# Performance work log

Hardware: AMD Instinct MI355X
Metric: run time of the kernel (lower is better)

The kernel has to match this reference:

```python
import jax, jax.numpy as jnp
from jax import lax
import numpy as np

L, B, D, H = 256, 128, 512, 512


def setup_inputs() -> dict:
    rng = np.random.default_rng(0)
    # random projective-ish dependency trees: node 0 is root, head[i] < i
    heads = np.full((B, L), -1, dtype=np.int64)
    for i in range(1, L):
        heads[:, i] = rng.integers(0, i, size=B)
    # bottom-up traversal order (children have larger index than parent)
    indexes = np.tile(np.arange(L - 1, -1, -1, dtype=np.int32)[:, None], (1, B))  # [L,B]
    # cm_full[b,p,j] = 1 if j is a child of p in tree b
    cm_full = (heads[:, None, :] == np.arange(L)[None, :, None]).astype(np.float32)  # [B,L,L]
    child_mask = cm_full[:, ::-1, :].transpose(1, 0, 2).copy()  # [L,B,L] aligned with indexes
    # top-down order: root first (ascending index works since head[i] < i)
    td_node = np.tile(np.arange(L, dtype=np.int32)[:, None], (1, B))  # [L,B]
    td_parent_idx = np.maximum(heads.T, 0).astype(np.int32)  # [L,B]
    td_parent_valid = (heads.T >= 0).astype(np.float32)  # [L,B], 0 at root
    root_index = np.zeros(B, dtype=np.int32)

    key = jax.random.key(0)
    ks = jax.random.split(key, 7)
    sx = 1.0 / np.sqrt(D)
    sh = 1.0 / np.sqrt(H)
    return {
        "emb": jax.random.normal(ks[0], (L, B, D), jnp.float32),
        "indexes": jnp.asarray(indexes),
        "child_mask": jnp.asarray(child_mask),
        "td_node": jnp.asarray(td_node),
        "td_parent_idx": jnp.asarray(td_parent_idx),
        "td_parent_valid": jnp.asarray(td_parent_valid),
        "root_index": jnp.asarray(root_index),
        "dt_Wx": jax.random.normal(ks[1], (D, 3 * H), jnp.float32) * sx,
        "dt_Uh": jax.random.normal(ks[2], (H, 3 * H), jnp.float32) * sh,
        "dt_b": jnp.zeros((3 * H,), jnp.float32),
        "td_Wx": jax.random.normal(ks[3], (D, 3 * H), jnp.float32) * sx,
        "td_Uh": jax.random.normal(ks[4], (H, 3 * H), jnp.float32) * sh,
        "td_b": jnp.zeros((3 * H,), jnp.float32),
    }


def _gru_cell(x, h, Wx, Uh, b):
    # standard GRU: gates laid out as [r, z, n]
    xg = x @ Wx + b
    hg = h @ Uh
    xr, xz, xn = jnp.split(xg, 3, axis=-1)
    hr, hz, hn = jnp.split(hg, 3, axis=-1)
    r = jax.nn.sigmoid(xr + hr)
    z = jax.nn.sigmoid(xz + hz)
    n = jnp.tanh(xn + r * hn)
    return (1.0 - z) * n + z * h


def reference(emb, indexes, child_mask, td_node, td_parent_idx, td_parent_valid,
              root_index, dt_Wx, dt_Uh, dt_b, td_Wx, td_Uh, td_b):
    Ld, Bd, Dd = emb.shape
    Hd = dt_Uh.shape[0]
    barange = jnp.arange(Bd)

    # ---- bottom-up (DT) pass: h_prev = sum of children hiddens ----
    x_dt = jnp.take_along_axis(emb, indexes[:, :, None], axis=0)  # [L,B,D]

    def dt_step(Hs, xs):
        x, node, cmask = xs                      # [B,D], [B], [B,L]
        h = jnp.einsum('bl,blh->bh', cmask, Hs)  # sum over children
        hn = _gru_cell(x, h, dt_Wx, dt_Uh, dt_b)
        return Hs.at[barange, node].set(hn), None

    Hdt, _ = lax.scan(dt_step, jnp.zeros((Bd, Ld, Hd), emb.dtype),
                      (x_dt, indexes, child_mask))

    # ---- top-down (TD) pass: h_prev = parent hidden (zeros at root) ----
    x_td = jnp.take_along_axis(emb, td_node[:, :, None], axis=0)  # [L,B,D]

    def td_step(Hs, xs):
        x, node, pidx, pvalid = xs
        h = Hs[barange, pidx] * pvalid[:, None]
        hn = _gru_cell(x, h, td_Wx, td_Uh, td_b)
        return Hs.at[barange, node].set(hn), None

    Htd, _ = lax.scan(td_step, jnp.zeros((Bd, Ld, Hd), emb.dtype),
                      (x_td, td_node, td_parent_idx, td_parent_valid))

    outputs = jnp.concatenate([Hdt, Htd], axis=-1)  # [B,L,2H] (batch-first as original)
    root_h = jnp.concatenate([Hdt[barange, root_index], Htd[barange, root_index]], axis=-1)
    output_t = root_h[None]  # [1,B,2H]
    return outputs, output_t
```

## Files before the change

kernel.cpp:

```cpp
#include <hip/hip_runtime.h>


#define NL 256
#define NB 128
#define NH 512
#define NG (NB * NL)

typedef short short8 __attribute__((ext_vector_type(8)));
typedef float f32x4 __attribute__((ext_vector_type(4)));

__device__ __forceinline__ float bf2f(unsigned short u) {
  union { unsigned int i; float f; } c; c.i = ((unsigned int)u) << 16; return c.f;
}
__device__ __forceinline__ unsigned short f2bf(float f) {
  union { float f; unsigned int i; } c; c.f = f;
  return (unsigned short)((c.i + 0x7FFFu + ((c.i >> 16) & 1u)) >> 16);
}
__device__ __forceinline__ short8 pk_bf16(f32x4 a, f32x4 b) {
  union { unsigned int u[4]; short8 s; } r;
  asm("v_cvt_pk_bf16_f32 %0, %1, %2" : "=v"(r.u[0]) : "v"(a[0]), "v"(a[1]));
  asm("v_cvt_pk_bf16_f32 %0, %1, %2" : "=v"(r.u[1]) : "v"(a[2]), "v"(a[3]));
  asm("v_cvt_pk_bf16_f32 %0, %1, %2" : "=v"(r.u[2]) : "v"(b[0]), "v"(b[1]));
  asm("v_cvt_pk_bf16_f32 %0, %1, %2" : "=v"(r.u[3]) : "v"(b[2]), "v"(b[3]));
  return r.s;
}
__device__ __forceinline__ void atom_pk_bf16(unsigned short* p, unsigned int ud) {
  asm volatile("global_atomic_pk_add_bf16 %0, %1, off" :: "v"((void*)p), "v"(ud) : "memory");
}

__device__ __forceinline__ void level_wait(unsigned int* c, unsigned int target) {
  if (threadIdx.x == 0) {
    while (__hip_atomic_load(c, __ATOMIC_RELAXED, __HIP_MEMORY_SCOPE_AGENT) < target)
      __builtin_amdgcn_s_sleep(8);
  }
  __syncthreads();
  __builtin_amdgcn_fence(__ATOMIC_ACQUIRE, "agent");
}

__global__ void prep_wt4(const float* __restrict__ w0, const float* __restrict__ w1,
                         const float* __restrict__ w2, const float* __restrict__ w3,
                         unsigned short* __restrict__ wt) {
  __shared__ float t[32][33];
  const float* w = blockIdx.z == 0 ? w0 : blockIdx.z == 1 ? w1 : blockIdx.z == 2 ? w2 : w3;
  unsigned short* dst = wt + (size_t)blockIdx.z * 1536 * 512;
  int n0 = blockIdx.x * 32, k0 = blockIdx.y * 32;
  int tx = threadIdx.x & 31, ty = threadIdx.x >> 5;
  #pragma unroll
  for (int i = 0; i < 4; ++i)
    t[ty + 8 * i][tx] = w[(size_t)(k0 + ty + 8 * i) * 1536 + n0 + tx];
  __syncthreads();
  #pragma unroll
  for (int i = 0; i < 4; ++i)
    dst[(size_t)(n0 + ty + 8 * i) * 512 + k0 + tx] = f2bf(t[tx][ty + 8 * i]);
}

__global__ void prep_sched(const int* __restrict__ td_pidx,
                           const float* __restrict__ td_pval,
                           int* __restrict__ sched, int* __restrict__ meta,
                           int* __restrict__ gidx, int* __restrict__ pslot) {
  __shared__ unsigned char dep[NB][NL];
  __shared__ unsigned short cnb[NB][256];
  __shared__ int cnt[256];
  __shared__ int off[257];
  __shared__ int dmax_s;
  const int tid = threadIdx.x;
  for (int j = tid; j < NB * 256; j += 256) ((unsigned short*)cnb)[j] = 0;
  if (tid == 0) dmax_s = 0;
  __syncthreads();
  if (tid < NB) {
    int b = tid, lmax = 0;
    for (int i = 0; i < NL; ++i) {
      float pv = td_pval[i * NB + b];
      int pi = td_pidx[i * NB + b];
      int d = (pv != 0.f) ? (int)dep[b][pi] + 1 : 0;
      dep[b][i] = (unsigned char)d;
      cnb[b][d]++;
      lmax = max(lmax, d);
    }
    atomicMax(&dmax_s, lmax);
  }
  __syncthreads();
  {
    int s = 0;
    for (int b = 0; b < NB; ++b) s += cnb[b][tid];
    cnt[tid] = s;
  }
  __syncthreads();
  if (tid == 0) {
    int s = 0;
    for (int d = 0; d < 256; ++d) { off[d] = s; s += cnt[d]; }
    off[256] = s;
  }
  __syncthreads();
  {
    int run = off[tid];
    for (int b = 0; b < NB; ++b) {
      int t = cnb[b][tid];
      cnb[b][tid] = (unsigned short)run;
      run += t;
    }
  }
  __syncthreads();
  if (tid < NB) {
    int b = tid;
    for (int i = 0; i < NL; ++i) {
      float pv = td_pval[i * NB + b];
      int pi = td_pidx[i * NB + b];
      int d = dep[b][i];
      int g = cnb[b][d]++;
      sched[g] = (b << 8) | i;
      gidx[b * NL + i] = g;
      pslot[g] = (pv != 0.f) ? gidx[b * NL + pi] : -1;
    }
  }
  if (tid == 0) meta[0] = dmax_s;
  __syncthreads();
  meta[1 + tid] = off[tid];
  meta[257 + tid] = cnt[tid];
}

__global__ void prep_xc(const float* __restrict__ emb, const int* __restrict__ sched,
                        unsigned short* __restrict__ Xc) {
  int g = blockIdx.x * 4 + (threadIdx.x >> 6);
  int lane = threadIdx.x & 63;
  int e = sched[g];
  int b = e >> 8, node = e & 255;
  const float* src = emb + ((size_t)node * NB + b) * 512 + lane * 8;
  f32x4 v0 = *(const f32x4*)src;
  f32x4 v1 = *(const f32x4*)(src + 4);
  *(short8*)(Xc + (size_t)g * 512 + lane * 8) = pk_bf16(v0, v1);
}

__launch_bounds__(512, 2)
__global__ void tree_gru(const float* __restrict__ dt_b,
                         const float* __restrict__ td_b,
                         const unsigned short* __restrict__ wt,
                         const unsigned short* __restrict__ Xc,
                         unsigned short* __restrict__ Hdt,
                         unsigned short* __restrict__ Htd,
                         unsigned short* __restrict__ Hfd,
                         const unsigned short* __restrict__ zrow,
                         const int* __restrict__ meta,
                         const int* __restrict__ pslot,
                         unsigned int* __restrict__ ctr,
                         const int* __restrict__ sched,
                         const int* __restrict__ root_index,
                         float* __restrict__ out) {
  extern __shared__ unsigned char lds[];
  const int tid = threadIdx.x;
  const int bi  = blockIdx.x;
  const int cg   = bi >> 3;
  const int pass = (bi >> 2) & 1;
  const int rep  = bi & 3;
  const int w  = tid >> 6, l = tid & 63;
  const int lm = l & 15, kg = l >> 4;
  const int col = cg * 16 + lm;

  for (int idx = tid; idx < 6144; idx += 512) {
    int k8  = idx & 63;
    int n   = (idx >> 6) & 15;
    int g   = (idx >> 10) % 3;
    int mat = idx / 3072;
    const unsigned short* src = wt + (size_t)(pass * 2 + mat) * (1536 * 512)
                                   + (size_t)(g * 512 + cg * 16 + n) * 512 + k8 * 8;
    short8 v = *(const short8*)src;
    int off = ((mat * 3 + g) * 16 + n) * 1024 + ((k8 * 16) ^ ((n & 7) << 4));
    *(short8*)(lds + off) = v;
  }
  unsigned char* Xb = lds + 98304;
  unsigned char* Hb = lds + 98304 + 16384;
  __syncthreads();

  const float* bias = pass ? td_b : dt_b;
  const float br = bias[col], bz = bias[NH + col], bn = bias[2 * NH + col];
  const int base_wr = (0 * 16 + lm) * 1024;
  const int base_wz = (1 * 16 + lm) * 1024;
  const int base_wn = (2 * 16 + lm) * 1024;
  const int base_ur = (3 * 16 + lm) * 1024;
  const int base_uz = (4 * 16 + lm) * 1024;
  const int base_un = (5 * 16 + lm) * 1024;
  const int wswz = (lm & 7) << 4;
  const int srow = tid >> 3, sslot = tid & 7;
  const int dsw = ((sslot ^ (srow & 7)) << 4);
  const int ck = cg >> 2;
  const int ccol2 = 2 * ((cg & 3) * 16 + lm);
  const int Dmax = meta[0];
  unsigned int* doneP = ctr + pass * 256;

  for (int p = 0; p <= Dmax; ++p) {
    const int d = pass ? p : (Dmax - p);
    const int off_d = meta[1 + d];
    const int cnt_d = meta[257 + d];
    const int T = (cnt_d + 127) >> 7;
    if (T <= rep) continue;
    const int dl = pass ? d - 1 : d + 1;
    if (dl >= 0 && dl <= Dmax)
      level_wait(doneP + dl, (unsigned int)meta[257 + dl] * 32u);
    for (int t = rep; t < T; t += 4) {
      const int g0 = off_d + t * 128;
      const int rows = min(128, cnt_d - t * 128);
      const unsigned short *sx[2], *sh[2];
      #pragma unroll
      for (int i = 0; i < 2; ++i) {
        int r = min(i * 64 + srow, rows - 1);
        int gg = g0 + r;
        sx[i] = Xc + (size_t)gg * 512 + sslot * 8;
        if (pass == 0) {
          sh[i] = Hdt + (size_t)gg * 512 + sslot * 8;
        } else {
          int ps = pslot[gg];
          sh[i] = (ps >= 0 ? Htd + (size_t)ps * 512 : zrow) + sslot * 8;
        }
      }
      const int c0 = (ck + 1) & 7;
      short8 rx0 = *(const short8*)(sx[0] + c0 * 64);
      short8 rx1 = *(const short8*)(sx[1] + c0 * 64);
      short8 rh0 = *(const short8*)(sh[0] + c0 * 64);
      short8 rh1 = *(const short8*)(sh[1] + c0 * 64);
      f32x4 aR = {0,0,0,0}, aZ = {0,0,0,0}, aXN = {0,0,0,0}, aHN = {0,0,0,0};
      #pragma unroll
      for (int ci = 0; ci < 8; ++ci) {
        const int c = (ck + 1 + ci) & 7;
        __syncthreads();
        *(short8*)(Xb + (srow)      * 128 + dsw) = rx0;
        *(short8*)(Xb + (64 + srow) * 128 + dsw) = rx1;
        *(short8*)(Hb + (srow)      * 128 + dsw) = rh0;
        *(short8*)(Hb + (64 + srow) * 128 + dsw) = rh1;
        if (ci < 7) {
          const int cn = (ck + 2 + ci) & 7;
          rx0 = *(const short8*)(sx[0] + cn * 64);
          rx1 = *(const short8*)(sx[1] + cn * 64);
          rh0 = *(const short8*)(sh[0] + cn * 64);
          rh1 = *(const short8*)(sh[1] + cn * 64);
        }
        __syncthreads();
        #pragma unroll
        for (int ks = 0; ks < 2; ++ks) {
          const int so = (((ks << 2) | kg) ^ (lm & 7)) << 4;
          const int arow = w * 16 + lm;
          short8 ax = *(const short8*)(Xb + arow * 128 + so);
          short8 ah = *(const short8*)(Hb + arow * 128 + so);
          const int kb = (c * 128 + ks * 64 + kg * 16) ^ wswz;
          short8 bwr = *(const short8*)(lds + base_wr + kb);
          short8 bwz = *(const short8*)(lds + base_wz + kb);
          short8 bwn = *(const short8*)(lds + base_wn + kb);
          short8 bur = *(const short8*)(lds + base_ur + kb);
          short8 buz = *(const short8*)(lds + base_uz + kb);
          short8 bun = *(const short8*)(lds + base_un + kb);
          aR  = __builtin_amdgcn_mfma_f32_16x16x32_bf16(ax, bwr, aR, 0, 0, 0);
          aZ  = __builtin_amdgcn_mfma_f32_16x16x32_bf16(ax, bwz, aZ, 0, 0, 0);
          aXN = __builtin_amdgcn_mfma_f32_16x16x32_bf16(ax, bwn, aXN, 0, 0, 0);
          aR  = __builtin_amdgcn_mfma_f32_16x16x32_bf16(ah, bur, aR, 0, 0, 0);
          aZ  = __builtin_amdgcn_mfma_f32_16x16x32_bf16(ah, buz, aZ, 0, 0, 0);
          aHN = __builtin_amdgcn_mfma_f32_16x16x32_bf16(ah, bun, aHN, 0, 0, 0);
        }
      }
      #pragma unroll
      for (int q = 0; q < 4; ++q) {
        const int r = w * 16 + kg * 4 + q;
        if (r >= rows) continue;
        const int g = g0 + r;
        const float hprev = bf2f(*(const unsigned short*)(
            Hb + r * 128 + (ccol2 ^ ((r & 7) << 4))));
        float rr = 1.f / (1.f + __expf(-(aR[q] + br)));
        float zz = 1.f / (1.f + __expf(-(aZ[q] + bz)));
        float e2 = __expf(2.f * (aXN[q] + bn + rr * aHN[q]));
        float nn = (e2 - 1.f) / (e2 + 1.f);
        float h = (1.f - zz) * nn + zz * hprev;
        float ho = __shfl_xor(h, 1);
        if (!(lm & 1)) {
          unsigned int ud;
          asm("v_cvt_pk_bf16_f32 %0, %1, %2" : "=v"(ud) : "v"(h), "v"(ho));
          if (pass == 0) {
            atom_pk_bf16(Hfd + (size_t)g * 512 + col, ud);
            int ps = pslot[g];
            if (ps >= 0) atom_pk_bf16(Hdt + (size_t)ps * 512 + col, ud);
          } else {
            atom_pk_bf16(Htd + (size_t)g * 512 + col, ud);
          }
        }
      }
      asm volatile("s_waitcnt vmcnt(0)" ::: "memory");
      __syncthreads();
      if (tid == 0) {
        __hip_atomic_fetch_add(doneP + d, (unsigned int)rows,
                               __ATOMIC_RELAXED, __HIP_MEMORY_SCOPE_AGENT);
        __hip_atomic_fetch_add(ctr + 512 + pass, (unsigned int)rows,
                               __ATOMIC_RELAXED, __HIP_MEMORY_SCOPE_AGENT);
      }
    }
  }

  level_wait(ctr + 512, (unsigned int)NG * 32u);
  level_wait(ctr + 513, (unsigned int)NG * 32u);
  #pragma unroll
  for (int it = 0; it < 4; ++it) {
    const int g = bi * 128 + it * 32 + (tid >> 4);
    const int part = tid & 15;
    const int e = sched[g];
    const int b = e >> 8, node = e & 255;
    float* dst = out + ((size_t)b * NL + node) * 1024;
    const bool isroot = (node == root_index[b]);
    float* dst2 = out + (size_t)NB * NL * 1024 + (size_t)b * 1024;
    const unsigned short* s1 = Hfd + (size_t)g * 512 + part * 32;
    const unsigned short* s2 = Htd + (size_t)g * 512 + part * 32;
    #pragma unroll
    for (int half = 0; half < 2; ++half) {
      const unsigned short* s = half ? s2 : s1;
      const int o = half * 512 + part * 32;
      #pragma unroll
      for (int j = 0; j < 4; ++j) {
        short8 v = *(const short8*)(s + j * 8);
        f32x4 lo, hi;
        #pragma unroll
        for (int q = 0; q < 4; ++q) {
          lo[q] = bf2f((unsigned short)v[q]);
          hi[q] = bf2f((unsigned short)v[4 + q]);
        }
        __builtin_nontemporal_store(lo, (f32x4*)(dst + o + j * 8));
        __builtin_nontemporal_store(hi, (f32x4*)(dst + o + j * 8 + 4));
        if (isroot) {
          *(f32x4*)(dst2 + o + j * 8) = lo;
          *(f32x4*)(dst2 + o + j * 8 + 4) = hi;
        }
      }
    }
  }
}

extern "C" void kernel_launch(void* const* d_in, const int* in_sizes, int n_in,
                              void* d_out, int out_size, void* d_ws, size_t ws_size,
                              hipStream_t stream) {
  (void)in_sizes; (void)n_in; (void)out_size; (void)ws_size;
  const float* emb      = (const float*)d_in[0];
  const int*   td_pidx  = (const int*)d_in[4];
  const float* td_pval  = (const float*)d_in[5];
  const int*   root_idx = (const int*)d_in[6];
  const float* dt_Wx    = (const float*)d_in[7];
  const float* dt_Uh    = (const float*)d_in[8];
  const float* dt_b     = (const float*)d_in[9];
  const float* td_Wx    = (const float*)d_in[10];
  const float* td_Uh    = (const float*)d_in[11];
  const float* td_b     = (const float*)d_in[12];
  float* out = (float*)d_out;

  unsigned short* wt   = (unsigned short*)d_ws;
  unsigned short* Xc   = wt + (size_t)4 * 1536 * 512;
  unsigned short* Hdt  = Xc + (size_t)NG * NH;
  unsigned short* Htd  = Hdt + (size_t)NG * NH;
  unsigned short* Hfd  = Htd + (size_t)NG * NH;
  unsigned short* zrow = Hfd + (size_t)NG * NH;
  unsigned int*   ctr  = (unsigned int*)(zrow + NH);
  int* sched = (int*)(ctr + 520);
  int* meta  = sched + NG;
  int* gidx  = meta + 520;
  int* pslot = gidx + NG;

  const size_t zbytes = (size_t)3 * NG * NH * 2 + NH * 2 + 520 * 4;
  (void)hipMemsetAsync(Hdt, 0, zbytes, stream);
  prep_wt4<<<dim3(48, 16, 4), dim3(256), 0, stream>>>(dt_Wx, dt_Uh, td_Wx, td_Uh, wt);
  prep_sched<<<dim3(1), dim3(256), 0, stream>>>(td_pidx, td_pval, sched, meta, gidx, pslot);
  prep_xc<<<dim3(NG / 4), dim3(256), 0, stream>>>(emb, sched, Xc);

  (void)hipFuncSetAttribute((const void*)tree_gru,
                            hipFuncAttributeMaxDynamicSharedMemorySize, 131072);

  void* args[] = {
    (void*)&dt_b, (void*)&td_b, (void*)&wt, (void*)&Xc, (void*)&Hdt, (void*)&Htd,
    (void*)&Hfd, (void*)&zrow, (void*)&meta, (void*)&pslot, (void*)&ctr,
    (void*)&sched, (void*)&root_idx, (void*)&out
  };
  (void)hipLaunchCooperativeKernel((const void*)tree_gru, dim3(256), dim3(512),
                                   args, 131072u, stream);
}
```

Before: 1.659 ms.

## Double row tile to 256 per block so each wave computes two MFMA row fragments

Raises the row tile per iteration from 128 to 256. Each wave now computes two 16-row fragments, which reuses every B-weight LDS read across twice as many MFMAs. Staging buffers grow to 32KB each and dynamic LDS rises to 160KB. Per-thread staging loads change to four 16-byte chunks per row-half, and the spin-wait sleep is shortened. In exchange, shallow levels have fewer tiles to spread across the 4 replicas per column group, so parallelism drops, and accumulator register use doubles.

```diff
diff --git a/kernel.cpp b/kernel.cpp
--- a/kernel.cpp
+++ b/kernel.cpp
@@ -31,7 +31,7 @@
 __device__ __forceinline__ void level_wait(unsigned int* c, unsigned int target) {
   if (threadIdx.x == 0) {
     while (__hip_atomic_load(c, __ATOMIC_RELAXED, __HIP_MEMORY_SCOPE_AGENT) < target)
-      __builtin_amdgcn_s_sleep(8);
+      __builtin_amdgcn_s_sleep(2);
   }
   __syncthreads();
   __builtin_amdgcn_fence(__ATOMIC_ACQUIRE, "agent");
@@ -168,7 +168,7 @@
     *(short8*)(lds + off) = v;
   }
   unsigned char* Xb = lds + 98304;
-  unsigned char* Hb = lds + 98304 + 16384;
+  unsigned char* Hb = lds + 98304 + 32768;
   __syncthreads();
 
   const float* bias = pass ? td_b : dt_b;
@@ -180,10 +180,11 @@
   const int base_uz = (4 * 16 + lm) * 1024;
   const int base_un = (5 * 16 + lm) * 1024;
   const int wswz = (lm & 7) << 4;
-  const int srow = tid >> 3, sslot = tid & 7;
-  const int dsw = ((sslot ^ (srow & 7)) << 4);
+  const int srow = tid >> 1;
+  const int shalf = (tid & 1) * 4;
   const int ck = cg >> 2;
-  const int ccol2 = 2 * ((cg & 3) * 16 + lm);
+  const int ccw = 2 * ((cg & 3) * 16 + lm);
+  const int ccslot = ccw >> 4, ccin = ccw & 15;
   const int Dmax = meta[0];
   unsigned int* doneP = ctr + pass * 256;
 
@@ -191,55 +192,64 @@
     const int d = pass ? p : (Dmax - p);
     const int off_d = meta[1 + d];
     const int cnt_d = meta[257 + d];
-    const int T = (cnt_d + 127) >> 7;
+    const int T = (cnt_d + 255) >> 8;
     if (T <= rep) continue;
     const int dl = pass ? d - 1 : d + 1;
     if (dl >= 0 && dl <= Dmax)
       level_wait(doneP + dl, (unsigned int)meta[257 + dl] * 32u);
     for (int t = rep; t < T; t += 4) {
-      const int g0 = off_d + t * 128;
-      const int rows = min(128, cnt_d - t * 128);
-      const unsigned short *sx[2], *sh[2];
-      #pragma unroll
-      for (int i = 0; i < 2; ++i) {
-        int r = min(i * 64 + srow, rows - 1);
-        int gg = g0 + r;
-        sx[i] = Xc + (size_t)gg * 512 + sslot * 8;
-        if (pass == 0) {
-          sh[i] = Hdt + (size_t)gg * 512 + sslot * 8;
-        } else {
-          int ps = pslot[gg];
-          sh[i] = (ps >= 0 ? Htd + (size_t)ps * 512 : zrow) + sslot * 8;
-        }
+      const int g0 = off_d + t * 256;
+      const int rows = min(256, cnt_d - t * 256);
+      const int gg = g0 + min(srow, rows - 1);
+      const unsigned short* sx = Xc + (size_t)gg * 512 + (tid & 1) * 32;
+      const unsigned short* sh;
+      if (pass == 0) {
+        sh = Hdt + (size_t)gg * 512 + (tid & 1) * 32;
+      } else {
+        int ps = pslot[gg];
+        sh = (ps >= 0 ? Htd + (size_t)ps * 512 : zrow) + (tid & 1) * 32;
       }
       const int c0 = (ck + 1) & 7;
-      short8 rx0 = *(const short8*)(sx[0] + c0 * 64);
-      short8 rx1 = *(const short8*)(sx[1] + c0 * 64);
-      short8 rh0 = *(const short8*)(sh[0] + c0 * 64);
-      short8 rh1 = *(const short8*)(sh[1] + c0 * 64);
-      f32x4 aR = {0,0,0,0}, aZ = {0,0,0,0}, aXN = {0,0,0,0}, aHN = {0,0,0,0};
+      short8 rx[4], rh[4];
+      #pragma unroll
+      for (int j = 0; j < 4; ++j) {
+        rx[j] = *(const short8*)(sx + c0 * 64 + j * 8);
+        rh[j] = *(const short8*)(sh + c0 * 64 + j * 8);
+      }
+      f32x4 aR[2], aZ[2], aXN[2], aHN[2];
+      #pragma unroll
+      for (int f = 0; f < 2; ++f) {
+        aR[f] = (f32x4){0,0,0,0}; aZ[f] = (f32x4){0,0,0,0};
+        aXN[f] = (f32x4){0,0,0,0}; aHN[f] = (f32x4){0,0,0,0};
+      }
       #pragma unroll
       for (int ci = 0; ci < 8; ++ci) {
         const int c = (ck + 1 + ci) & 7;
         __syncthreads();
-        *(short8*)(Xb + (srow)      * 128 + dsw) = rx0;
-        *(short8*)(Xb + (64 + srow) * 128 + dsw) = rx1;
-        *(short8*)(Hb + (srow)      * 128 + dsw) = rh0;
-        *(short8*)(Hb + (64 + srow) * 128 + dsw) = rh1;
+        #pragma unroll
+        for (int j = 0; j < 4; ++j) {
+          const int so = ((shalf + j) ^ (srow & 7)) << 4;
+          *(short8*)(Xb + srow * 128 + so) = rx[j];
+          *(short8*)(Hb + srow * 128 + so) = rh[j];
+        }
         if (ci < 7) {
           const int cn = (ck + 2 + ci) & 7;
-          rx0 = *(const short8*)(sx[0] + cn * 64);
-          rx1 = *(const short8*)(sx[1] + cn * 64);
-          rh0 = *(const short8*)(sh[0] + cn * 64);
-          rh1 = *(const short8*)(sh[1] + cn * 64);
+          #pragma unroll
+          for (int j = 0; j < 4; ++j) {
+            rx[j] = *(const short8*)(sx + cn * 64 + j * 8);
+            rh[j] = *(const short8*)(sh + cn * 64 + j * 8);
+          }
         }
         __syncthreads();
         #pragma unroll
         for (int ks = 0; ks < 2; ++ks) {
           const int so = (((ks << 2) | kg) ^ (lm & 7)) << 4;
-          const int arow = w * 16 + lm;
-          short8 ax = *(const short8*)(Xb + arow * 128 + so);
-          short8 ah = *(const short8*)(Hb + arow * 128 + so);
+          const int r0 = (w * 32 + lm) * 128;
+          const int r1 = (w * 32 + 16 + lm) * 128;
+          short8 ax0 = *(const short8*)(Xb + r0 + so);
+          short8 ax1 = *(const short8*)(Xb + r1 + so);
+          short8 ah0 = *(const short8*)(Hb + r0 + so);
+          short8 ah1 = *(const short8*)(Hb + r1 + so);
           const int kb = (c * 128 + ks * 64 + kg * 16) ^ wswz;
           short8 bwr = *(const short8*)(lds + base_wr + kb);
           short8 bwz = *(const short8*)(lds + base_wz + kb);
@@ -247,24 +257,31 @@
           short8 bur = *(const short8*)(lds + base_ur + kb);
           short8 buz = *(const short8*)(lds + base_uz + kb);
           short8 bun = *(const short8*)(lds + base_un + kb);
-          aR  = __builtin_amdgcn_mfma_f32_16x16x32_bf16(ax, bwr, aR, 0, 0, 0);
-          aZ  = __builtin_amdgcn_mfma_f32_16x16x32_bf16(ax, bwz, aZ, 0, 0, 0);
-          aXN = __builtin_amdgcn_mfma_f32_16x16x32_bf16(ax, bwn, aXN, 0, 0, 0);
-          aR  = __builtin_amdgcn_mfma_f32_16x16x32_bf16(ah, bur, aR, 0, 0, 0);
-          aZ  = __builtin_amdgcn_mfma_f32_16x16x32_bf16(ah, buz, aZ, 0, 0, 0);
-          aHN = __builtin_amdgcn_mfma_f32_16x16x32_bf16(ah, bun, aHN, 0, 0, 0);
-        }
-      }
-      #pragma unroll
-      for (int q = 0; q < 4; ++q) {
-        const int r = w * 16 + kg * 4 + q;
+          aR[0]  = __builtin_amdgcn_mfma_f32_16x16x32_bf16(ax0, bwr, aR[0], 0, 0, 0);
+          aR[1]  = __builtin_amdgcn_mfma_f32_16x16x32_bf16(ax1, bwr, aR[1], 0, 0, 0);
+          aZ[0]  = __builtin_amdgcn_mfma_f32_16x16x32_bf16(ax0, bwz, aZ[0], 0, 0, 0);
+          aZ[1]  = __builtin_amdgcn_mfma_f32_16x16x32_bf16(ax1, bwz, aZ[1], 0, 0, 0);
+          aXN[0] = __builtin_amdgcn_mfma_f32_16x16x32_bf16(ax0, bwn, aXN[0], 0, 0, 0);
+          aXN[1] = __builtin_amdgcn_mfma_f32_16x16x32_bf16(ax1, bwn, aXN[1], 0, 0, 0);
+          aR[0]  = __builtin_amdgcn_mfma_f32_16x16x32_bf16(ah0, bur, aR[0], 0, 0, 0);
+          aR[1]  = __builtin_amdgcn_mfma_f32_16x16x32_bf16(ah1, bur, aR[1], 0, 0, 0);
+          aZ[0]  = __builtin_amdgcn_mfma_f32_16x16x32_bf16(ah0, buz, aZ[0], 0, 0, 0);
+          aZ[1]  = __builtin_amdgcn_mfma_f32_16x16x32_bf16(ah1, buz, aZ[1], 0, 0, 0);
+          aHN[0] = __builtin_amdgcn_mfma_f32_16x16x32_bf16(ah0, bun, aHN[0], 0, 0, 0);
+          aHN[1] = __builtin_amdgcn_mfma_f32_16x16x32_bf16(ah1, bun, aHN[1], 0, 0, 0);
+        }
+      }
+      #pragma unroll
+      for (int fq = 0; fq < 8; ++fq) {
+        const int f = fq >> 2, q = fq & 3;
+        const int r = w * 32 + f * 16 + kg * 4 + q;
         if (r >= rows) continue;
         const int g = g0 + r;
         const float hprev = bf2f(*(const unsigned short*)(
-            Hb + r * 128 + (ccol2 ^ ((r & 7) << 4))));
-        float rr = 1.f / (1.f + __expf(-(aR[q] + br)));
-        float zz = 1.f / (1.f + __expf(-(aZ[q] + bz)));
-        float e2 = __expf(2.f * (aXN[q] + bn + rr * aHN[q]));
+            Hb + r * 128 + (((ccslot ^ (r & 7)) << 4) | ccin)));
+        float rr = 1.f / (1.f + __expf(-(aR[f][q] + br)));
+        float zz = 1.f / (1.f + __expf(-(aZ[f][q] + bz)));
+        float e2 = __expf(2.f * (aXN[f][q] + bn + rr * aHN[f][q]));
         float nn = (e2 - 1.f) / (e2 + 1.f);
         float h = (1.f - zz) * nn + zz * hprev;
         float ho = __shfl_xor(h, 1);
@@ -363,7 +380,7 @@
   prep_xc<<<dim3(NG / 4), dim3(256), 0, stream>>>(emb, sched, Xc);
 
   (void)hipFuncSetAttribute((const void*)tree_gru,
-                            hipFuncAttributeMaxDynamicSharedMemorySize, 131072);
+                            hipFuncAttributeMaxDynamicSharedMemorySize, 163840);
 
   void* args[] = {
     (void*)&dt_b, (void*)&td_b, (void*)&wt, (void*)&Xc, (void*)&Hdt, (void*)&Htd,
@@ -371,5 +388,5 @@
     (void*)&sched, (void*)&root_idx, (void*)&out
   };
   (void)hipLaunchCooperativeKernel((const void*)tree_gru, dim3(256), dim3(512),
-                                   args, 131072u, stream);
-}
+                                   args, 163840u, stream);
+}
```

Result: no change. 1.680 ms (+1.2%).

## Double-buffer LDS staging, prefetch next tile, and batch level-completion signals

Applied to the files above, without the earlier changes.

The X/H staging is now double-buffered in LDS, so each k-chunk needs one barrier instead of two, and the next chunk is prefetched while the MFMAs run. The first chunks of the next tile are loaded before the current tile's results are written out. Per-row atomic adds for Hfd/Htd become write-through plain stores, and the done-counters are bumped once per level instead of once per tile. The spin sleep is shortened, and the acquire fence is dropped, leaning on sc0/sc1 write-through stores and a custom non-temporal zero kernel. LDS grows to 160KB, and removing the fence risks reading stale cached data across XCDs.

```diff
diff --git a/kernel.cpp b/kernel.cpp
--- a/kernel.cpp
+++ b/kernel.cpp
@@ -27,14 +27,26 @@
 __device__ __forceinline__ void atom_pk_bf16(unsigned short* p, unsigned int ud) {
   asm volatile("global_atomic_pk_add_bf16 %0, %1, off" :: "v"((void*)p), "v"(ud) : "memory");
 }
+__device__ __forceinline__ void store_u32_wt(unsigned short* p, unsigned int v) {
+  asm volatile("global_store_dword %0, %1, off sc0 sc1" :: "v"((void*)p), "v"(v) : "memory");
+}
 
 __device__ __forceinline__ void level_wait(unsigned int* c, unsigned int target) {
   if (threadIdx.x == 0) {
     while (__hip_atomic_load(c, __ATOMIC_RELAXED, __HIP_MEMORY_SCOPE_AGENT) < target)
-      __builtin_amdgcn_s_sleep(8);
-  }
-  __syncthreads();
-  __builtin_amdgcn_fence(__ATOMIC_ACQUIRE, "agent");
+      __builtin_amdgcn_s_sleep(2);
+  }
+  __syncthreads();
+}
+
+__global__ void prep_zero(f32x4* __restrict__ base, int n16) {
+  const f32x4 z = {0.f, 0.f, 0.f, 0.f};
+  int i = blockIdx.x * blockDim.x + threadIdx.x;
+  int stride = gridDim.x * blockDim.x;
+  for (int j = i; j < n16; j += stride) {
+    asm volatile("global_store_dwordx4 %0, %1, off sc0 sc1 nt"
+                 :: "v"((void*)(base + j)), "v"(z) : "memory");
+  }
 }
 
 __global__ void prep_wt4(const float* __restrict__ w0, const float* __restrict__ w1,
@@ -130,6 +142,18 @@
   f32x4 v1 = *(const f32x4*)(src + 4);
   *(short8*)(Xc + (size_t)g * 512 + lane * 8) = pk_bf16(v0, v1);
 }
+
+#define LDJ(j, rx, rh)                                            \
+  { const int c_ = (ck + 1 + (j)) & 7;                            \
+    rx[0] = *(const short8*)(sx + c_ * 64);                       \
+    rx[1] = *(const short8*)(sx + c_ * 64 + 8);                   \
+    rh[0] = *(const short8*)(sh + c_ * 64);                       \
+    rh[1] = *(const short8*)(sh + c_ * 64 + 8); }
+#define WRB(Xp, Hp, rx, rh)                                       \
+  { *(short8*)((Xp) + srow * 128 + sw0) = rx[0];                  \
+    *(short8*)((Xp) + srow * 128 + sw1) = rx[1];                  \
+    *(short8*)((Hp) + srow * 128 + sw0) = rh[0];                  \
+    *(short8*)((Hp) + srow * 128 + sw1) = rh[1]; }
 
 __launch_bounds__(512, 2)
 __global__ void tree_gru(const float* __restrict__ dt_b,
@@ -167,8 +191,10 @@
     int off = ((mat * 3 + g) * 16 + n) * 1024 + ((k8 * 16) ^ ((n & 7) << 4));
     *(short8*)(lds + off) = v;
   }
-  unsigned char* Xb = lds + 98304;
-  unsigned char* Hb = lds + 98304 + 16384;
+  unsigned char* Xb0 = lds + 98304;
+  unsigned char* Hb0 = Xb0 + 16384;
+  unsigned char* Xb1 = Hb0 + 16384;
+  unsigned char* Hb1 = Xb1 + 16384;
   __syncthreads();
 
   const float* bias = pass ? td_b : dt_b;
@@ -180,10 +206,12 @@
   const int base_uz = (4 * 16 + lm) * 1024;
   const int base_un = (5 * 16 + lm) * 1024;
   const int wswz = (lm & 7) << 4;
-  const int srow = tid >> 3, sslot = tid & 7;
-  const int dsw = ((sslot ^ (srow & 7)) << 4);
+  const int srow = tid >> 2, sq = tid & 3;
+  const int sw0 = ((sq * 2)     ^ (srow & 7)) << 4;
+  const int sw1 = ((sq * 2 + 1) ^ (srow & 7)) << 4;
   const int ck = cg >> 2;
-  const int ccol2 = 2 * ((cg & 3) * 16 + lm);
+  const int ccw = 2 * ((cg & 3) * 16 + lm);
+  const int ccslot = ccw >> 4, ccin = ccw & 15;
   const int Dmax = meta[0];
   unsigned int* doneP = ctr + pass * 256;
 
@@ -196,50 +224,39 @@
     const int dl = pass ? d - 1 : d + 1;
     if (dl >= 0 && dl <= Dmax)
       level_wait(doneP + dl, (unsigned int)meta[257 + dl] * 32u);
+
+    unsigned int myrows = 0;
+    const unsigned short *sx, *sh;
+    {
+      const int gg = off_d + min(rep * 128 + srow, cnt_d - 1);
+      sx = Xc + (size_t)gg * 512 + sq * 16;
+      if (pass == 0) sh = Hdt + (size_t)gg * 512 + sq * 16;
+      else { int ps = pslot[gg]; sh = (ps >= 0 ? Htd + (size_t)ps * 512 : zrow) + sq * 16; }
+    }
+    short8 x0[2], h0[2], x1[2], h1[2];
+    LDJ(0, x0, h0);
+    LDJ(1, x1, h1);
+
     for (int t = rep; t < T; t += 4) {
       const int g0 = off_d + t * 128;
       const int rows = min(128, cnt_d - t * 128);
-      const unsigned short *sx[2], *sh[2];
-      #pragma unroll
-      for (int i = 0; i < 2; ++i) {
-        int r = min(i * 64 + srow, rows - 1);
-        int gg = g0 + r;
-        sx[i] = Xc + (size_t)gg * 512 + sslot * 8;
-        if (pass == 0) {
-          sh[i] = Hdt + (size_t)gg * 512 + sslot * 8;
-        } else {
-          int ps = pslot[gg];
-          sh[i] = (ps >= 0 ? Htd + (size_t)ps * 512 : zrow) + sslot * 8;
-        }
-      }
-      const int c0 = (ck + 1) & 7;
-      short8 rx0 = *(const short8*)(sx[0] + c0 * 64);
-      short8 rx1 = *(const short8*)(sx[1] + c0 * 64);
-      short8 rh0 = *(const short8*)(sh[0] + c0 * 64);
-      short8 rh1 = *(const short8*)(sh[1] + c0 * 64);
+      __syncthreads();
+      WRB(Xb0, Hb0, x0, h0);
+      LDJ(2, x0, h0);
+      __syncthreads();
+
       f32x4 aR = {0,0,0,0}, aZ = {0,0,0,0}, aXN = {0,0,0,0}, aHN = {0,0,0,0};
       #pragma unroll
       for (int ci = 0; ci < 8; ++ci) {
         const int c = (ck + 1 + ci) & 7;
-        __syncthreads();
-        *(short8*)(Xb + (srow)      * 128 + dsw) = rx0;
-        *(short8*)(Xb + (64 + srow) * 128 + dsw) = rx1;
-        *(short8*)(Hb + (srow)      * 128 + dsw) = rh0;
-        *(short8*)(Hb + (64 + srow) * 128 + dsw) = rh1;
-        if (ci < 7) {
-          const int cn = (ck + 2 + ci) & 7;
-          rx0 = *(const short8*)(sx[0] + cn * 64);
-          rx1 = *(const short8*)(sx[1] + cn * 64);
-          rh0 = *(const short8*)(sh[0] + cn * 64);
-          rh1 = *(const short8*)(sh[1] + cn * 64);
-        }
-        __syncthreads();
+        const unsigned char* Ax = (ci & 1) ? Xb1 : Xb0;
+        const unsigned char* Ah = (ci & 1) ? Hb1 : Hb0;
         #pragma unroll
         for (int ks = 0; ks < 2; ++ks) {
           const int so = (((ks << 2) | kg) ^ (lm & 7)) << 4;
-          const int arow = w * 16 + lm;
-          short8 ax = *(const short8*)(Xb + arow * 128 + so);
-          short8 ah = *(const short8*)(Hb + arow * 128 + so);
+          const int ar = (w * 16 + lm) * 128;
+          short8 ax = *(const short8*)(Ax + ar + so);
+          short8 ah = *(const short8*)(Ah + ar + so);
           const int kb = (c * 128 + ks * 64 + kg * 16) ^ wswz;
           short8 bwr = *(const short8*)(lds + base_wr + kb);
           short8 bwz = *(const short8*)(lds + base_wz + kb);
@@ -254,40 +271,66 @@
           aZ  = __builtin_amdgcn_mfma_f32_16x16x32_bf16(ah, buz, aZ, 0, 0, 0);
           aHN = __builtin_amdgcn_mfma_f32_16x16x32_bf16(ah, bun, aHN, 0, 0, 0);
         }
+        if (ci < 7) {
+          unsigned char* Wx = (ci & 1) ? Xb0 : Xb1;
+          unsigned char* Wh = (ci & 1) ? Hb0 : Hb1;
+          if ((ci & 1) == 0) {
+            WRB(Wx, Wh, x1, h1);
+            if (ci < 5) LDJ(ci + 3, x1, h1);
+          } else {
+            WRB(Wx, Wh, x0, h0);
+            if (ci < 5) LDJ(ci + 3, x0, h0);
+          }
+          __syncthreads();
+        }
+      }
+      float hv[4];
+      #pragma unroll
+      for (int q = 0; q < 4; ++q) {
+        const int r = w * 16 + kg * 4 + q;
+        const float hprev = bf2f(*(const unsigned short*)(
+            Hb1 + r * 128 + (((ccslot ^ (r & 7)) << 4) | ccin)));
+        float rr = 1.f / (1.f + __expf(-(aR[q] + br)));
+        float zz = 1.f / (1.f + __expf(-(aZ[q] + bz)));
+        float e2 = __expf(2.f * (aXN[q] + bn + rr * aHN[q]));
+        float nn = (e2 - 1.f) / (e2 + 1.f);
+        hv[q] = (1.f - zz) * nn + zz * hprev;
+      }
+      if (t + 4 < T) {
+        const int gg = off_d + min((t + 4) * 128 + srow, cnt_d - 1);
+        sx = Xc + (size_t)gg * 512 + sq * 16;
+        if (pass == 0) sh = Hdt + (size_t)gg * 512 + sq * 16;
+        else { int ps = pslot[gg]; sh = (ps >= 0 ? Htd + (size_t)ps * 512 : zrow) + sq * 16; }
+        LDJ(0, x0, h0);
+        LDJ(1, x1, h1);
       }
       #pragma unroll
       for (int q = 0; q < 4; ++q) {
         const int r = w * 16 + kg * 4 + q;
         if (r >= rows) continue;
         const int g = g0 + r;
-        const float hprev = bf2f(*(const unsigned short*)(
-            Hb + r * 128 + (ccol2 ^ ((r & 7) << 4))));
-        float rr = 1.f / (1.f + __expf(-(aR[q] + br)));
-        float zz = 1.f / (1.f + __expf(-(aZ[q] + bz)));
-        float e2 = __expf(2.f * (aXN[q] + bn + rr * aHN[q]));
-        float nn = (e2 - 1.f) / (e2 + 1.f);
-        float h = (1.f - zz) * nn + zz * hprev;
-        float ho = __shfl_xor(h, 1);
+        float ho = __shfl_xor(hv[q], 1);
         if (!(lm & 1)) {
           unsigned int ud;
-          asm("v_cvt_pk_bf16_f32 %0, %1, %2" : "=v"(ud) : "v"(h), "v"(ho));
+          asm("v_cvt_pk_bf16_f32 %0, %1, %2" : "=v"(ud) : "v"(hv[q]), "v"(ho));
           if (pass == 0) {
-            atom_pk_bf16(Hfd + (size_t)g * 512 + col, ud);
+            store_u32_wt(Hfd + (size_t)g * 512 + col, ud);
             int ps = pslot[g];
             if (ps >= 0) atom_pk_bf16(Hdt + (size_t)ps * 512 + col, ud);
           } else {
-            atom_pk_bf16(Htd + (size_t)g * 512 + col, ud);
+            store_u32_wt(Htd + (size_t)g * 512 + col, ud);
           }
         }
       }
-      asm volatile("s_waitcnt vmcnt(0)" ::: "memory");
-      __syncthreads();
-      if (tid == 0) {
-        __hip_atomic_fetch_add(doneP + d, (unsigned int)rows,
-                               __ATOMIC_RELAXED, __HIP_MEMORY_SCOPE_AGENT);
-        __hip_atomic_fetch_add(ctr + 512 + pass, (unsigned int)rows,
-                               __ATOMIC_RELAXED, __HIP_MEMORY_SCOPE_AGENT);
-      }
+      myrows += (unsigned int)rows;
+    }
+    asm volatile("s_waitcnt vmcnt(0)" ::: "memory");
+    __syncthreads();
+    if (tid == 0) {
+      __hip_atomic_fetch_add(doneP + d, myrows,
+                             __ATOMIC_RELAXED, __HIP_MEMORY_SCOPE_AGENT);
+      __hip_atomic_fetch_add(ctr + 512 + pass, myrows,
+                             __ATOMIC_RELAXED, __HIP_MEMORY_SCOPE_AGENT);
     }
   }
 
@@ -356,14 +399,14 @@
   int* gidx  = meta + 520;
   int* pslot = gidx + NG;
 
-  const size_t zbytes = (size_t)3 * NG * NH * 2 + NH * 2 + 520 * 4;
-  (void)hipMemsetAsync(Hdt, 0, zbytes, stream);
+  const int n16 = (int)(((size_t)3 * NG * NH * 2 + NH * 2 + 520 * 4) / 16);
+  prep_zero<<<dim3(2048), dim3(256), 0, stream>>>((f32x4*)Hdt, n16);
   prep_wt4<<<dim3(48, 16, 4), dim3(256), 0, stream>>>(dt_Wx, dt_Uh, td_Wx, td_Uh, wt);
   prep_sched<<<dim3(1), dim3(256), 0, stream>>>(td_pidx, td_pval, sched, meta, gidx, pslot);
   prep_xc<<<dim3(NG / 4), dim3(256), 0, stream>>>(emb, sched, Xc);
 
   (void)hipFuncSetAttribute((const void*)tree_gru,
-                            hipFuncAttributeMaxDynamicSharedMemorySize, 131072);
+                            hipFuncAttributeMaxDynamicSharedMemorySize, 163840);
 
   void* args[] = {
     (void*)&dt_b, (void*)&td_b, (void*)&wt, (void*)&Xc, (void*)&Hdt, (void*)&Htd,
@@ -371,5 +414,5 @@
     (void*)&sched, (void*)&root_idx, (void*)&out
   };
   (void)hipLaunchCooperativeKernel((const void*)tree_gru, dim3(256), dim3(512),
-                                   args, 131072u, stream);
-}
+                                   args, 163840u, stream);
+}
```

Result: faster. 1.398 ms (-15.7%).
